# Kernel optimization log

Hardware: AMD Instinct MI355X
Metric: run time of the kernel (lower is better)

Reference implementation:

```python
import jax, jax.numpy as jnp
import numpy as np
from math import exp

C1 = 0.01 ** 2
C2 = 0.03 ** 2
WINDOW_SIZE = 11
SIGMA = 1.5

def make_window(window_size, channel, sigma=SIGMA):
    g = np.array([exp(-(x - window_size // 2) ** 2 / float(2 * sigma ** 2))
                  for x in range(window_size)], dtype=np.float32)
    g = g / g.sum()
    w2d = np.outer(g, g).astype(np.float32)  # [ws, ws]
    # depthwise kernel, OIHW with I=1 per group: [C, 1, ws, ws]
    return jnp.asarray(np.broadcast_to(w2d, (channel, 1, window_size, window_size)).copy())

def depthwise_conv(x, window, pad):
    C = x.shape[1]
    return jax.lax.conv_general_dilated(
        x, window, window_strides=(1, 1),
        padding=[(pad, pad), (pad, pad)],
        feature_group_count=C,
        dimension_numbers=('NCHW', 'OIHW', 'NCHW'))

def setup_inputs() -> dict:
    key = jax.random.key(0)
    k1, k2 = jax.random.split(key)
    B, C, H, W = 16, 3, 512, 512
    img1 = jax.random.uniform(k1, (B, C, H, W), dtype=jnp.float32)
    img2 = jax.random.uniform(k2, (B, C, H, W), dtype=jnp.float32)
    window = make_window(WINDOW_SIZE, C)
    return {"img1": img1, "img2": img2, "window": window}

def reference(img1, img2, window):
    pad = WINDOW_SIZE // 2
    mu1 = depthwise_conv(img1, window, pad)
    mu2 = depthwise_conv(img2, window, pad)
    mu1_sq = mu1 * mu1
    mu2_sq = mu2 * mu2
    mu1_mu2 = mu1 * mu2
    sigma1_sq = depthwise_conv(img1 * img1, window, pad) - mu1_sq
    sigma2_sq = depthwise_conv(img2 * img2, window, pad) - mu2_sq
    sigma12 = depthwise_conv(img1 * img2, window, pad) - mu1_mu2
    ssim_cs = (2 * sigma12 + C2) / (sigma1_sq + sigma2_sq + C2)
    ssim_l = (2 * mu1_mu2 + C1) / (mu1_sq + mu2_sq + C1)
    ssim_map = ssim_l * ssim_cs
    return jnp.mean(ssim_map)
```

## Files before the change

kernel.cpp:

```cpp
#include <hip/hip_runtime.h>


typedef float v2f __attribute__((ext_vector_type(2)));

#define IMG_H 512
#define IMG_W 512
#define N_IMG 48
#define WS 11
#define PAD 5
#define CHUNK 16
#define NCHUNK (IMG_H / CHUNK)
#define RING 14
#define PLANE_B 5248
#define INV_NPX (1.0f / (48.0f * 512.0f * 512.0f))

__device__ __forceinline__ unsigned swz8(int E) {
    return (unsigned)((E + (E >> 2)) * 8);
}
__device__ __forceinline__ v2f vfma(v2f a, v2f b, v2f c) {
    return __builtin_elementwise_fma(a, b, c);
}

__global__ __launch_bounds__(256, 3) void ssim_partial_kernel(
    const float* __restrict__ img1,
    const float* __restrict__ img2,
    const float* __restrict__ window,
    float* __restrict__ out)
{
    __shared__ __align__(16) char lds[8 * PLANE_B];
    __shared__ float wred[4];

    const int tid = threadIdx.x;
    const int bc  = blockIdx.x;
    const int r0  = blockIdx.y * CHUNK;
    const int col = tid * 2;

    float g[WS];
    {
        const float g5  = sqrtf(window[5 * WS + 5]);
        const float inv = 1.0f / g5;
#pragma unroll
        for (int j = 0; j < WS; ++j) g[j] = window[5 * WS + j] * inv;
    }
    const float C1v = 0.01f * 0.01f;
    const float C2v = 0.03f * 0.03f;

    const float* __restrict__ p1 = img1 + (size_t)bc * (IMG_H * IMG_W);
    const float* __restrict__ p2 = img2 + (size_t)bc * (IMG_H * IMG_W);

    const unsigned woffA = swz8(col + 6);
    const unsigned woffB = swz8(col + 7);
    const int q  = tid & 127;
    const int jj = tid >> 7;
    unsigned roff[14];
#pragma unroll
    for (int m = 0; m < 14; ++m) roff[m] = swz8(4 * q + 1 + m);

    if (tid < 96) {
        const int pj = tid / 12, h = tid % 12;
        const int E  = (h < 6) ? h : (512 + h);
        *(v2f*)(lds + pj * PLANE_B + swz8(E)) = (v2f)(0.0f);
    }
    __syncthreads();

    v2f rx1[RING], rx2[RING];
#pragma unroll
    for (int i = 0; i < RING; ++i) { rx1[i] = (v2f)(0.0f); rx2[i] = (v2f)(0.0f); }

#pragma unroll
    for (int i = 0; i < 10; ++i) {
        const int rr = r0 - PAD + i;
        v2f u1 = (v2f)(0.0f), u2 = (v2f)(0.0f);
        if (rr >= 0 && rr < IMG_H) {
            u1 = *(const v2f*)(p1 + rr * IMG_W + col);
            u2 = *(const v2f*)(p2 + rr * IMG_W + col);
        }
        rx1[4 + i] = u1; rx2[4 + i] = u2;
    }

    float acc = 0.0f;

    for (int step = 0; step < CHUNK / 4; ++step) {
        const int R = r0 + step * 4;

#pragma unroll
        for (int i = 0; i < RING - 4; ++i) { rx1[i] = rx1[i + 4]; rx2[i] = rx2[i + 4]; }
#pragma unroll
        for (int j = 0; j < 4; ++j) {
            const int rr = R + PAD + j;
            v2f u1 = (v2f)(0.0f), u2 = (v2f)(0.0f);
            if (rr < IMG_H) {
                u1 = *(const v2f*)(p1 + rr * IMG_W + col);
                u2 = *(const v2f*)(p2 + rr * IMG_W + col);
            }
            rx1[10 + j] = u1; rx2[10 + j] = u2;
        }

        v2f va[4][4];
#pragma unroll
        for (int p = 0; p < 4; ++p)
#pragma unroll
            for (int k = 0; k < 4; ++k) va[p][k] = (v2f)(0.0f);
#pragma unroll
        for (int k = 0; k < 4; ++k) {
#pragma unroll
            for (int i = 0; i < WS; ++i) {
                const v2f w  = (v2f)(g[i]);
                const v2f X1 = rx1[i + k], X2 = rx2[i + k];
                va[0][k] = vfma(w, X1, va[0][k]);
                va[1][k] = vfma(w, X2, va[1][k]);
                va[2][k] = vfma(w, vfma(X1, X1, X2 * X2), va[2][k]);
                va[3][k] = vfma(w, X1 * X2, va[3][k]);
            }
        }
#pragma unroll
        for (int jp = 0; jp < 2; ++jp) {
#pragma unroll
            for (int p = 0; p < 4; ++p) {
                char* base = lds + (jp * 4 + p) * PLANE_B;
                *(v2f*)(base + woffA) = (v2f){va[p][2 * jp].x, va[p][2 * jp + 1].x};
                *(v2f*)(base + woffB) = (v2f){va[p][2 * jp].y, va[p][2 * jp + 1].y};
            }
        }
        __syncthreads();

        v2f h[4][4];
#pragma unroll
        for (int p = 0; p < 4; ++p) {
            const char* base = lds + (jj * 4 + p) * PLANE_B;
            v2f r[14];
#pragma unroll
            for (int m = 0; m < 14; ++m) r[m] = *(const v2f*)(base + roff[m]);
#pragma unroll
            for (int d = 0; d < 4; ++d) {
                v2f s = (v2f)(0.0f);
#pragma unroll
                for (int i = 0; i < WS; ++i) s = vfma((v2f)(g[i]), r[d + i], s);
                h[p][d] = s;
            }
        }
#pragma unroll
        for (int d = 0; d < 4; ++d) {
            const v2f mu1 = h[0][d], mu2 = h[1][d];
            const v2f hs  = h[2][d], hp  = h[3][d];
            const v2f mu1s = mu1 * mu1;
            const v2f mu2s = mu2 * mu2;
            const v2f mu12 = mu1 * mu2;
            const v2f sgs  = hs - mu1s - mu2s;
            const v2f sg12 = hp - mu12;
            const v2f num  = (2.f * mu12 + (v2f)(C1v)) * (2.f * sg12 + (v2f)(C2v));
            const v2f den  = (mu1s + mu2s + (v2f)(C1v)) * (sgs + (v2f)(C2v));
            v2f r = {__builtin_amdgcn_rcpf(den.x), __builtin_amdgcn_rcpf(den.y)};
            r = r * vfma(-den, r, (v2f)(2.0f));
            acc = fmaf(num.x, r.x, acc);
            acc = fmaf(num.y, r.y, acc);
        }
        __syncthreads();
    }

#pragma unroll
    for (int off = 32; off > 0; off >>= 1)
        acc += __shfl_down(acc, off);
    if ((tid & 63) == 0) wred[tid >> 6] = acc;
    __syncthreads();
    if (tid == 0) {
        const float s = (wred[0] + wred[1]) + (wred[2] + wred[3]);
        atomicAdd(out, s * INV_NPX);
    }
}

extern "C" void kernel_launch(void* const* d_in, const int* in_sizes, int n_in,
                              void* d_out, int out_size, void* d_ws, size_t ws_size,
                              hipStream_t stream) {
    const float* img1   = (const float*)d_in[0];
    const float* img2   = (const float*)d_in[1];
    const float* window = (const float*)d_in[2];
    float* out = (float*)d_out;

    hipMemsetAsync(out, 0, sizeof(float), stream);
    dim3 grid(N_IMG, NCHUNK);
    ssim_partial_kernel<<<grid, 256, 0, stream>>>(img1, img2, window, out);
}
```

Measured before the change: 136.3 us.

## Process two output rows per step with prefetched loads and higher occupancy

Each step now computes two output rows instead of four. This shrinks the register ring, the accumulators and the LDS staging to half. Launch bounds go from 3 to 6 waves-per-EU occupancy, and the next two input rows are loaded into pending registers one step early so global loads overlap compute. The step loop is fully unrolled and the final barrier is skipped. The trade-off is twice as many barriers and LDS round trips per chunk, and the horizontal pass now has 11/2 taps of overlap reuse instead of 11/4.

```diff
diff --git a/kernel.cpp b/kernel.cpp
--- a/kernel.cpp
+++ b/kernel.cpp
@@ -10,7 +10,7 @@
 #define PAD 5
 #define CHUNK 16
 #define NCHUNK (IMG_H / CHUNK)
-#define RING 14
+#define RING 12
 #define PLANE_B 5248
 #define INV_NPX (1.0f / (48.0f * 512.0f * 512.0f))
 
@@ -21,13 +21,13 @@
     return __builtin_elementwise_fma(a, b, c);
 }
 
-__global__ __launch_bounds__(256, 3) void ssim_partial_kernel(
+__global__ __launch_bounds__(256, 6) void ssim_partial_kernel(
     const float* __restrict__ img1,
     const float* __restrict__ img2,
     const float* __restrict__ window,
     float* __restrict__ out)
 {
-    __shared__ __align__(16) char lds[8 * PLANE_B];
+    __shared__ __align__(16) char lds[4 * PLANE_B];
     __shared__ float wred[4];
 
     const int tid = threadIdx.x;
@@ -50,13 +50,11 @@
 
     const unsigned woffA = swz8(col + 6);
     const unsigned woffB = swz8(col + 7);
-    const int q  = tid & 127;
-    const int jj = tid >> 7;
-    unsigned roff[14];
+    unsigned roff[12];
 #pragma unroll
-    for (int m = 0; m < 14; ++m) roff[m] = swz8(4 * q + 1 + m);
+    for (int m = 0; m < 12; ++m) roff[m] = swz8(col + 1 + m);
 
-    if (tid < 96) {
+    if (tid < 48) {
         const int pj = tid / 12, h = tid % 12;
         const int E  = (h < 6) ? h : (512 + h);
         *(v2f*)(lds + pj * PLANE_B + swz8(E)) = (v2f)(0.0f);
@@ -75,34 +73,51 @@
             u1 = *(const v2f*)(p1 + rr * IMG_W + col);
             u2 = *(const v2f*)(p2 + rr * IMG_W + col);
         }
-        rx1[4 + i] = u1; rx2[4 + i] = u2;
+        rx1[2 + i] = u1; rx2[2 + i] = u2;
+    }
+    v2f pend1[2], pend2[2];
+#pragma unroll
+    for (int j = 0; j < 2; ++j) {
+        const int rr = r0 + PAD + j;
+        v2f u1 = (v2f)(0.0f), u2 = (v2f)(0.0f);
+        if (rr < IMG_H) {
+            u1 = *(const v2f*)(p1 + rr * IMG_W + col);
+            u2 = *(const v2f*)(p2 + rr * IMG_W + col);
+        }
+        pend1[j] = u1; pend2[j] = u2;
     }
 
     float acc = 0.0f;
 
-    for (int step = 0; step < CHUNK / 4; ++step) {
-        const int R = r0 + step * 4;
+#pragma unroll
+    for (int step = 0; step < CHUNK / 2; ++step) {
+        const int R = r0 + step * 2;
 
 #pragma unroll
-        for (int i = 0; i < RING - 4; ++i) { rx1[i] = rx1[i + 4]; rx2[i] = rx2[i + 4]; }
+        for (int i = 0; i < RING - 2; ++i) { rx1[i] = rx1[i + 2]; rx2[i] = rx2[i + 2]; }
+        rx1[10] = pend1[0]; rx2[10] = pend2[0];
+        rx1[11] = pend1[1]; rx2[11] = pend2[1];
+
+        if (step + 1 < CHUNK / 2) {
 #pragma unroll
-        for (int j = 0; j < 4; ++j) {
-            const int rr = R + PAD + j;
-            v2f u1 = (v2f)(0.0f), u2 = (v2f)(0.0f);
-            if (rr < IMG_H) {
-                u1 = *(const v2f*)(p1 + rr * IMG_W + col);
-                u2 = *(const v2f*)(p2 + rr * IMG_W + col);
+            for (int j = 0; j < 2; ++j) {
+                const int rr = R + 7 + j;
+                v2f u1 = (v2f)(0.0f), u2 = (v2f)(0.0f);
+                if (rr < IMG_H) {
+                    u1 = *(const v2f*)(p1 + rr * IMG_W + col);
+                    u2 = *(const v2f*)(p2 + rr * IMG_W + col);
+                }
+                pend1[j] = u1; pend2[j] = u2;
             }
-            rx1[10 + j] = u1; rx2[10 + j] = u2;
         }
 
-        v2f va[4][4];
+        v2f va[4][2];
 #pragma unroll
         for (int p = 0; p < 4; ++p)
 #pragma unroll
-            for (int k = 0; k < 4; ++k) va[p][k] = (v2f)(0.0f);
+            for (int k = 0; k < 2; ++k) va[p][k] = (v2f)(0.0f);
 #pragma unroll
-        for (int k = 0; k < 4; ++k) {
+        for (int k = 0; k < 2; ++k) {
 #pragma unroll
             for (int i = 0; i < WS; ++i) {
                 const v2f w  = (v2f)(g[i]);
@@ -114,25 +129,22 @@
             }
         }
 #pragma unroll
-        for (int jp = 0; jp < 2; ++jp) {
-#pragma unroll
-            for (int p = 0; p < 4; ++p) {
-                char* base = lds + (jp * 4 + p) * PLANE_B;
-                *(v2f*)(base + woffA) = (v2f){va[p][2 * jp].x, va[p][2 * jp + 1].x};
-                *(v2f*)(base + woffB) = (v2f){va[p][2 * jp].y, va[p][2 * jp + 1].y};
-            }
+        for (int p = 0; p < 4; ++p) {
+            char* base = lds + p * PLANE_B;
+            *(v2f*)(base + woffA) = (v2f){va[p][0].x, va[p][1].x};
+            *(v2f*)(base + woffB) = (v2f){va[p][0].y, va[p][1].y};
         }
         __syncthreads();
 
-        v2f h[4][4];
+        v2f h[4][2];
 #pragma unroll
         for (int p = 0; p < 4; ++p) {
-            const char* base = lds + (jj * 4 + p) * PLANE_B;
-            v2f r[14];
+            const char* base = lds + p * PLANE_B;
+            v2f r[12];
 #pragma unroll
-            for (int m = 0; m < 14; ++m) r[m] = *(const v2f*)(base + roff[m]);
+            for (int m = 0; m < 12; ++m) r[m] = *(const v2f*)(base + roff[m]);
 #pragma unroll
-            for (int d = 0; d < 4; ++d) {
+            for (int d = 0; d < 2; ++d) {
                 v2f s = (v2f)(0.0f);
 #pragma unroll
                 for (int i = 0; i < WS; ++i) s = vfma((v2f)(g[i]), r[d + i], s);
@@ -140,7 +152,7 @@
             }
         }
 #pragma unroll
-        for (int d = 0; d < 4; ++d) {
+        for (int d = 0; d < 2; ++d) {
             const v2f mu1 = h[0][d], mu2 = h[1][d];
             const v2f hs  = h[2][d], hp  = h[3][d];
             const v2f mu1s = mu1 * mu1;
@@ -155,7 +167,7 @@
             acc = fmaf(num.x, r.x, acc);
             acc = fmaf(num.y, r.y, acc);
         }
-        __syncthreads();
+        if (step + 1 < CHUNK / 2) __syncthreads();
     }
 
 #pragma unroll
```

Result: slower. 529.8 us (+288.6%).
